# Kernel optimization log

Hardware: AMD Instinct MI355X
Metric: run time of the kernel (lower is better)

The kernel has to match this reference:

```python
import jax, jax.numpy as jnp
import numpy as np

HEADS = 16
DIM = 1024
D_K = DIM // HEADS
SEQ = 2048


def setup_inputs() -> dict:
    key = jax.random.key(0)
    ks = jax.random.split(key, 11)
    s = 1.0 / np.sqrt(DIM).astype(np.float32)
    return {
        "q": jax.random.normal(ks[0], (SEQ, DIM), jnp.float32),
        "k": jax.random.normal(ks[1], (SEQ, DIM), jnp.float32),
        "v": jax.random.normal(ks[2], (SEQ, DIM), jnp.float32),
        "Wq": jax.random.normal(ks[3], (DIM, DIM), jnp.float32) * s,
        "bq": jax.random.normal(ks[4], (DIM,), jnp.float32) * 0.01,
        "Wk": jax.random.normal(ks[5], (DIM, DIM), jnp.float32) * s,
        "bk": jax.random.normal(ks[6], (DIM,), jnp.float32) * 0.01,
        "Wv": jax.random.normal(ks[7], (DIM, DIM), jnp.float32) * s,
        "bv": jax.random.normal(ks[8], (DIM,), jnp.float32) * 0.01,
        "Wo": jax.random.normal(ks[9], (DIM, DIM), jnp.float32) * s,
        "bo": jax.random.normal(ks[10], (DIM,), jnp.float32) * 0.01,
    }


def reference(q, k, v, Wq, bq, Wk, bk, Wv, bv, Wo, bo):
    S = q.shape[0]
    # torch Linear: x @ W.T + b; view to (1, S, H, d_k) then transpose to (1, H, S, d_k)
    def proj(x, W, b):
        return (x @ W.T + b).reshape(1, S, HEADS, D_K).transpose(0, 2, 1, 3)

    qh = proj(q, Wq, bq)  # (1, H, S, d)
    kh = proj(k, Wk, bk)
    vh = proj(v, Wv, bv)

    scale = 1.0 / np.sqrt(D_K).astype(np.float32)
    scores = jnp.einsum("bhqd,bhkd->bhqk", qh, kh) * scale  # (1, H, S, S)
    # NOTE: source applies softmax over dim=1 == the HEADS axis (faithful quirk)
    attn = jax.nn.softmax(scores, axis=1)
    ctx = jnp.einsum("bhqk,bhkd->bhqd", attn, vh)  # (1, H, S, d)
    concat = ctx.transpose(0, 2, 1, 3).reshape(1, S, DIM)
    return concat @ Wo.T + bo
```

## Files before the change

kernel.cpp:

```cpp
#include <hip/hip_runtime.h>
#include <hip/hip_fp16.h>


typedef _Float16 f16;
typedef _Float16 f16x4 __attribute__((ext_vector_type(4)));
typedef _Float16 f16x8 __attribute__((ext_vector_type(8)));
typedef float    f32x4 __attribute__((ext_vector_type(4)));

#define S_LEN 2048
#define DIM   1024
#define NH    16
#define DK    64
#define EXP2K 0.1803368801111244f

#define MFMA(a, b, c) __builtin_amdgcn_mfma_f32_16x16x32_f16(a, b, c, 0, 0, 0)

#define VM_WAIT0   asm volatile("s_waitcnt vmcnt(0)" ::: "memory")
#define LGKM_WAIT0 asm volatile("s_waitcnt lgkmcnt(0)" ::: "memory")
#define WG_BARRIER asm volatile("s_barrier" ::: "memory")

typedef __attribute__((address_space(1))) void g_void;
typedef __attribute__((address_space(3))) void l_void;

static __device__ __forceinline__ void gload_lds16(const void* g, void* l) {
  __builtin_amdgcn_global_load_lds((g_void*)g, (l_void*)l, 16, 0, 0);
}

static __device__ __forceinline__ float exp_s(float s) {
  return __builtin_amdgcn_exp2f(s * EXP2K);
}

__global__ __launch_bounds__(256) void cvt_all(
    const float* __restrict__ q, const float* __restrict__ k, const float* __restrict__ v,
    const float* __restrict__ Wq, const float* __restrict__ Wk, const float* __restrict__ Wv,
    const float* __restrict__ Wo, f16* __restrict__ qh, f16* __restrict__ kh,
    f16* __restrict__ vh, f16* __restrict__ wqh, f16* __restrict__ wkh,
    f16* __restrict__ wvh, f16* __restrict__ woh) {
  const size_t M = 1048576;
  const int seg = blockIdx.y;
  const float* src;
  f16* dst;
  switch (seg) {
    case 0: src = q;      dst = qh;      break;
    case 1: src = q + M;  dst = qh + M;  break;
    case 2: src = k;      dst = kh;      break;
    case 3: src = k + M;  dst = kh + M;  break;
    case 4: src = v;      dst = vh;      break;
    case 5: src = v + M;  dst = vh + M;  break;
    case 6: src = Wq;     dst = wqh;     break;
    case 7: src = Wk;     dst = wkh;     break;
    case 8: src = Wv;     dst = wvh;     break;
    default: src = Wo;    dst = woh;     break;
  }
  int i = blockIdx.x * 256 + threadIdx.x;
  float4 vv = ((const float4*)src)[i];
  f16x4 o = {(f16)vv.x, (f16)vv.y, (f16)vv.z, (f16)vv.w};
  ((f16x4*)dst)[i] = o;
}

static __device__ __forceinline__ void gemm64_core(const f16* __restrict__ X,
                                                   const f16* __restrict__ W,
                                                   int bm, int bn,
                                                   f16* As, f16* Bs,
                                                   f32x4 (&acc)[4][2]) {
  const int tid = threadIdx.x;
  const int wv = tid >> 6;
  const int lane = tid & 63;
  const int qd = lane >> 4;
  const int l16 = lane & 15;
  const int wm = (wv & 1) * 64;
  const int wn = (wv >> 1) * 32;
  const int lr8 = lane >> 3, lc8 = lane & 7;
  const int l7 = l16 & 7;

  const f16* gA = X + (size_t)(bm + wv * 32 + lr8) * DIM + (lc8 ^ lr8) * 8;
  const f16* gB = W + (size_t)(bn + wv * 16 + lr8) * DIM + (lc8 ^ lr8) * 8;

  auto issue = [&](int t, f16* dA, f16* dB) {
#pragma unroll
    for (int g = 0; g < 4; g++)
      gload_lds16(gA + (size_t)(g * 8) * DIM + t * 64, dA + (wv * 32 + g * 8) * 64);
#pragma unroll
    for (int g = 0; g < 2; g++)
      gload_lds16(gB + (size_t)(g * 8) * DIM + t * 64, dB + (wv * 16 + g * 8) * 64);
  };

  issue(0, As, Bs);

#pragma unroll 2
  for (int t = 0; t < 16; t++) {
    const int buf = t & 1;
    VM_WAIT0;
    WG_BARRIER;
    if (t + 1 < 16)
      issue(t + 1, As + (buf ^ 1) * (128 * 64), Bs + (buf ^ 1) * (64 * 64));
    const f16* A = As + buf * (128 * 64);
    const f16* B = Bs + buf * (64 * 64);
#pragma unroll
    for (int kk = 0; kk < 2; kk++) {
      const int slot = ((kk * 4 + qd) ^ l7) * 8;
      f16x8 bf[2];
#pragma unroll
      for (int ni = 0; ni < 2; ni++)
        bf[ni] = *(const f16x8*)&B[(wn + ni * 16 + l16) * 64 + slot];
#pragma unroll
      for (int mi = 0; mi < 4; mi++) {
        f16x8 af = *(const f16x8*)&A[(wm + mi * 16 + l16) * 64 + slot];
#pragma unroll
        for (int ni = 0; ni < 2; ni++)
          acc[mi][ni] = MFMA(af, bf[ni], acc[mi][ni]);
      }
    }
  }
}

__global__ __launch_bounds__(256) void gemm_qkv(
    const f16* __restrict__ X0, const f16* __restrict__ X1, const f16* __restrict__ X2,
    const f16* __restrict__ W0, const f16* __restrict__ W1, const f16* __restrict__ W2,
    const float* __restrict__ b0, const float* __restrict__ b1, const float* __restrict__ b2,
    f16* __restrict__ o0, f16* __restrict__ o1, f16* __restrict__ o2) {
  __shared__ __align__(16) f16 As[2 * 128 * 64];
  __shared__ __align__(16) f16 Bs[2 * 64 * 64];
  const int z = blockIdx.z;
  const f16* X = z == 0 ? X0 : z == 1 ? X1 : X2;
  const f16* W = z == 0 ? W0 : z == 1 ? W1 : W2;
  const float* bias = z == 0 ? b0 : z == 1 ? b1 : b2;
  f16* outh = z == 0 ? o0 : z == 1 ? o1 : o2;

  const int bm = blockIdx.y * 128, bn = blockIdx.x * 64;
  f32x4 acc[4][2];
#pragma unroll
  for (int a = 0; a < 4; a++)
#pragma unroll
    for (int b = 0; b < 2; b++) acc[a][b] = (f32x4){0.f, 0.f, 0.f, 0.f};

  gemm64_core(X, W, bm, bn, As, Bs, acc);

  const int tid = threadIdx.x;
  const int wv = tid >> 6, lane = tid & 63;
  const int qd = lane >> 4, l16 = lane & 15;
  const int wm = (wv & 1) * 64, wn = (wv >> 1) * 32;
#pragma unroll
  for (int mi = 0; mi < 4; mi++) {
#pragma unroll
    for (int ni = 0; ni < 2; ni++) {
      const int gm = bm + wm + mi * 16 + qd * 4;
      const int gn = bn + wn + ni * 16 + l16;
      const float bs = bias[gn];
      if (z == 2) {
        f16x4 o = {(f16)(acc[mi][ni][0] + bs), (f16)(acc[mi][ni][1] + bs),
                   (f16)(acc[mi][ni][2] + bs), (f16)(acc[mi][ni][3] + bs)};
        const int pj = (gm & ~31) + ((gm >> 2) & 3) * 8 + ((gm >> 4) & 1) * 4;
        *(f16x4*)&outh[(size_t)gn * S_LEN + pj] = o;
      } else {
#pragma unroll
        for (int r = 0; r < 4; r++)
          outh[(size_t)(gm + r) * DIM + gn] = (f16)(acc[mi][ni][r] + bs);
      }
    }
  }
}

__global__ __launch_bounds__(256) void gemm_out(const f16* __restrict__ C0,
                                                const f16* __restrict__ C1,
                                                const f16* __restrict__ W,
                                                const float* __restrict__ bias,
                                                float* __restrict__ outf) {
  __shared__ __align__(16) f16 As[2 * 64 * 64];
  __shared__ __align__(16) f16 Bs[2 * 64 * 64];
  const int tid = threadIdx.x;
  const int wv = tid >> 6;
  const int lane = tid & 63;
  const int qd = lane >> 4;
  const int l16 = lane & 15;
  const int wm = (wv & 1) * 32;
  const int wn = (wv >> 1) * 32;
  const int lr8 = lane >> 3, lc8 = lane & 7;
  const int l7 = l16 & 7;
  const int bm = blockIdx.y * 64, bn = blockIdx.x * 64;

  const f16* gA0 = C0 + (size_t)(bm + wv * 16 + lr8) * DIM + lc8 * 8;
  const f16* gA1 = C1 + (size_t)(bm + wv * 16 + lr8) * DIM + lc8 * 8;
  const f16* gB  = W + (size_t)(bn + wv * 16 + lr8) * DIM + (lc8 ^ lr8) * 8;

  f16x8 a0[2], a1[2];
  auto issueA = [&](int t) {
#pragma unroll
    for (int g = 0; g < 2; g++) {
      a0[g] = *(const f16x8*)(gA0 + (size_t)(g * 8) * DIM + t * 64);
      a1[g] = *(const f16x8*)(gA1 + (size_t)(g * 8) * DIM + t * 64);
    }
  };
  auto issueB = [&](int t, f16* dB) {
#pragma unroll
    for (int g = 0; g < 2; g++)
      gload_lds16(gB + (size_t)(g * 8) * DIM + t * 64, dB + (wv * 16 + g * 8) * 64);
  };

  f32x4 acc[2][2];
#pragma unroll
  for (int a = 0; a < 2; a++)
#pragma unroll
    for (int b = 0; b < 2; b++) acc[a][b] = (f32x4){0.f, 0.f, 0.f, 0.f};

  issueA(0);
  issueB(0, Bs);

#pragma unroll 2
  for (int t = 0; t < 16; t++) {
    const int buf = t & 1;
    VM_WAIT0;
    f16* Ab = As + buf * (64 * 64);
#pragma unroll
    for (int g = 0; g < 2; g++) {
      f16x8 s;
#pragma unroll
      for (int j = 0; j < 8; j++) s[j] = (f16)((float)a0[g][j] + (float)a1[g][j]);
      *(f16x8*)&Ab[(wv * 16 + g * 8 + lr8) * 64 + (lc8 ^ lr8) * 8] = s;
    }
    LGKM_WAIT0;
    WG_BARRIER;
    if (t + 1 < 16) {
      issueA(t + 1);
      issueB(t + 1, Bs + (buf ^ 1) * (64 * 64));
    }
    const f16* A = Ab;
    const f16* B = Bs + buf * (64 * 64);
#pragma unroll
    for (int kk = 0; kk < 2; kk++) {
      const int slot = ((kk * 4 + qd) ^ l7) * 8;
      f16x8 bf[2], af[2];
#pragma unroll
      for (int ni = 0; ni < 2; ni++)
        bf[ni] = *(const f16x8*)&B[(wn + ni * 16 + l16) * 64 + slot];
#pragma unroll
      for (int mi = 0; mi < 2; mi++)
        af[mi] = *(const f16x8*)&A[(wm + mi * 16 + l16) * 64 + slot];
#pragma unroll
      for (int mi = 0; mi < 2; mi++)
#pragma unroll
        for (int ni = 0; ni < 2; ni++)
          acc[mi][ni] = MFMA(af[mi], bf[ni], acc[mi][ni]);
    }
  }

#pragma unroll
  for (int mi = 0; mi < 2; mi++) {
#pragma unroll
    for (int ni = 0; ni < 2; ni++) {
      const int gm = bm + wm + mi * 16 + qd * 4;
      const int gn = bn + wn + ni * 16 + l16;
      const float bs = bias[gn];
#pragma unroll
      for (int r = 0; r < 4; r++)
        outf[(size_t)(gm + r) * DIM + gn] = acc[mi][ni][r] + bs;
    }
  }
}

__global__ __launch_bounds__(256) void attn_denom(const f16* __restrict__ Qp,
                                                  const f16* __restrict__ Kp,
                                                  f16* __restrict__ IDn) {
  __shared__ __align__(16) f16 Qs[2][2][64 * 32];
  __shared__ __align__(16) f16 Ks[2][2][64 * 32];
  const int tid = threadIdx.x;
  const int wv = tid >> 6;
  const int lane = tid & 63;
  const int qd = lane >> 4;
  const int l16 = lane & 15;
  const int wm = (wv & 1) * 32, wn = (wv >> 1) * 32;
  const int flat = blockIdx.x + (blockIdx.y << 5);
  const int nf = ((flat & 7) << 7) + (flat >> 3);
  const int bi = (nf >> 5) * 64, bj = (nf & 31) * 64;
  const int lr4 = lane >> 2, lc4 = lane & 3;
  const int kkw = wv & 1;
  const int q0 = (wv >> 1) * 2;
  const int ssw = (lc4 ^ ((lr4 >> 1) & 3)) * 8;
  const int rsw = (qd ^ ((l16 >> 1) & 3)) * 8;

  f32x4 dsum[2][2];
#pragma unroll
  for (int a = 0; a < 2; a++)
#pragma unroll
    for (int b = 0; b < 2; b++) dsum[a][b] = (f32x4){0.f, 0.f, 0.f, 0.f};

  {
    const f16* gq = Qp + (size_t)(bi + q0 * 16 + lr4) * DIM + kkw * 32 + ssw;
    const f16* gk = Kp + (size_t)(bj + q0 * 16 + lr4) * DIM + kkw * 32 + ssw;
#pragma unroll
    for (int t = 0; t < 2; t++) {
      gload_lds16(gq + (size_t)t * 16 * DIM, &Qs[0][kkw][(q0 + t) * 16 * 32]);
      gload_lds16(gk + (size_t)t * 16 * DIM, &Ks[0][kkw][(q0 + t) * 16 * 32]);
    }
  }

#pragma unroll 2
  for (int h = 0; h < NH; h++) {
    const int buf = h & 1;
    VM_WAIT0;
    WG_BARRIER;
    if (h + 1 < NH) {
      const f16* gq = Qp + (size_t)(bi + q0 * 16 + lr4) * DIM + (h + 1) * DK + kkw * 32 + ssw;
      const f16* gk = Kp + (size_t)(bj + q0 * 16 + lr4) * DIM + (h + 1) * DK + kkw * 32 + ssw;
#pragma unroll
      for (int t = 0; t < 2; t++) {
        gload_lds16(gq + (size_t)t * 16 * DIM, &Qs[buf ^ 1][kkw][(q0 + t) * 16 * 32]);
        gload_lds16(gk + (size_t)t * 16 * DIM, &Ks[buf ^ 1][kkw][(q0 + t) * 16 * 32]);
      }
    }

#pragma unroll
    for (int mi = 0; mi < 2; mi++) {
      f16x8 af0 = *(const f16x8*)&Qs[buf][0][(wm + mi * 16 + l16) * 32 + rsw];
      f16x8 af1 = *(const f16x8*)&Qs[buf][1][(wm + mi * 16 + l16) * 32 + rsw];
#pragma unroll
      for (int ni = 0; ni < 2; ni++) {
        f16x8 bf0 = *(const f16x8*)&Ks[buf][0][(wn + ni * 16 + l16) * 32 + rsw];
        f16x8 bf1 = *(const f16x8*)&Ks[buf][1][(wn + ni * 16 + l16) * 32 + rsw];
        f32x4 s = {0.f, 0.f, 0.f, 0.f};
        s = MFMA(af0, bf0, s);
        s = MFMA(af1, bf1, s);
#pragma unroll
        for (int r = 0; r < 4; r++) dsum[mi][ni][r] += exp_s(s[r]);
      }
    }
  }
#pragma unroll
  for (int mi = 0; mi < 2; mi++)
#pragma unroll
    for (int ni = 0; ni < 2; ni++)
#pragma unroll
      for (int r = 0; r < 4; r++) {
        const int gi = bi + wm + mi * 16 + qd * 4 + r;
        const int gj = bj + wn + ni * 16 + l16;
        const int pj = (gj & ~31) + ((gj >> 2) & 3) * 8 + ((gj >> 4) & 1) * 4 + (gj & 3);
        IDn[(size_t)gi * S_LEN + pj] = (f16)(1.f / dsum[mi][ni][r]);
      }
}

__global__ __launch_bounds__(256, 4) void attn_ctx(const f16* __restrict__ Qp,
                                                   const f16* __restrict__ Kp,
                                                   const f16* __restrict__ Vt,
                                                   const f16* __restrict__ IDn,
                                                   f16* __restrict__ C0,
                                                   f16* __restrict__ C1) {
  __shared__ __align__(16) f16 Ks[2][2][64 * 32];
  __shared__ __align__(16) f16 Vs[2][64 * 64];
  const int tid = threadIdx.x;
  const int wv = tid >> 6;
  const int lane = tid & 63;
  const int qd = lane >> 4;
  const int l16 = lane & 15;
  const int flat = blockIdx.x + (blockIdx.y << 5) + (blockIdx.z << 9);
  const int nf = ((flat & 7) << 7) + (flat >> 3);
  const int h = (nf >> 5) & 15;
  const int iw = (nf & 31) * 64 + wv * 16;
  const int z = nf >> 9;
  const int jb = z * 1024;
  f16* Cz = z == 0 ? C0 : C1;
  const int lr4 = lane >> 2, lc4 = lane & 3;
  const int lr8 = lane >> 3, lc8 = lane & 7;
  const int kkw = wv & 1;
  const int rhw = wv >> 1;
  const int ssw = (lc4 ^ ((lr4 >> 1) & 3)) * 8;
  const int rsw = (qd ^ ((l16 >> 1) & 3)) * 8;
  const int l7 = l16 & 7;

  f16x8 aq[2];
#pragma unroll
  for (int kk = 0; kk < 2; kk++)
    aq[kk] = *(const f16x8*)(Qp + (size_t)(iw + l16) * DIM + h * DK + kk * 32 + qd * 8);

  f32x4 acc[4];
#pragma unroll
  for (int b = 0; b < 4; b++) acc[b] = (f32x4){0.f, 0.f, 0.f, 0.f};

  f16x8 idn[2][2];

  auto issue = [&](int tt, int pb) {
    const int j1 = jb + tt * 64;
    const f16* gk = Kp + (size_t)(j1 + rhw * 16 + lr4) * DIM + h * DK + kkw * 32 + ssw;
    gload_lds16(gk, &Ks[pb][kkw][(rhw * 16) * 32]);
    gload_lds16(gk + (size_t)32 * DIM, &Ks[pb][kkw][(rhw * 16 + 32) * 32]);
    const f16* gv = Vt + (size_t)(h * DK + wv * 16 + lr8) * S_LEN + j1 + (lc8 ^ lr8) * 8;
    gload_lds16(gv, &Vs[pb][(wv * 16) * 64]);
    gload_lds16(gv + (size_t)8 * S_LEN, &Vs[pb][(wv * 16 + 8) * 64]);
#pragma unroll
    for (int js = 0; js < 2; js++)
      idn[pb][js] = *(const f16x8*)(IDn + (size_t)(iw + l16) * S_LEN + j1 + js * 32 + qd * 8);
  };

  issue(0, 0);

#pragma unroll 2
  for (int t = 0; t < 16; t++) {
    const int buf = t & 1;
    VM_WAIT0;
    WG_BARRIER;
    if (t + 1 < 16) issue(t + 1, buf ^ 1);

    f16x8 pa[2];
#pragma unroll
    for (int js = 0; js < 2; js++) {
      f16x8 bk0[2], bk1[2];
#pragma unroll
      for (int kk = 0; kk < 2; kk++) {
        bk0[kk] = *(const f16x8*)&Ks[buf][kk][((js * 2) * 16 + l16) * 32 + rsw];
        bk1[kk] = *(const f16x8*)&Ks[buf][kk][((js * 2 + 1) * 16 + l16) * 32 + rsw];
      }
      f32x4 st0 = {0.f, 0.f, 0.f, 0.f};
      f32x4 st1 = {0.f, 0.f, 0.f, 0.f};
      st0 = MFMA(bk0[0], aq[0], st0);
      st0 = MFMA(bk0[1], aq[1], st0);
      st1 = MFMA(bk1[0], aq[0], st1);
      st1 = MFMA(bk1[1], aq[1], st1);
      f16x8 p;
#pragma unroll
      for (int r = 0; r < 4; r++) p[r] = (f16)(exp_s(st0[r]) * (float)idn[buf][js][r]);
#pragma unroll
      for (int r = 0; r < 4; r++) p[4 + r] = (f16)(exp_s(st1[r]) * (float)idn[buf][js][4 + r]);
      pa[js] = p;
    }

#pragma unroll
    for (int js = 0; js < 2; js++) {
#pragma unroll
      for (int nd = 0; nd < 4; nd++) {
        f16x8 bv = *(const f16x8*)&Vs[buf][(nd * 16 + l16) * 64 +
                                          (((js * 4 + qd) ^ l7) * 8)];
        acc[nd] = MFMA(pa[js], bv, acc[nd]);
      }
    }
  }

#pragma unroll
  for (int nd = 0; nd < 4; nd++)
#pragma unroll
    for (int r = 0; r < 4; r++)
      Cz[(size_t)(iw + qd * 4 + r) * DIM + h * DK + nd * 16 + l16] = (f16)acc[nd][r];
}

extern "C" void kernel_launch(void* const* d_in, const int* in_sizes, int n_in,
                              void* d_out, int out_size, void* d_ws, size_t ws_size,
                              hipStream_t stream) {
  const float* q  = (const float*)d_in[0];
  const float* k  = (const float*)d_in[1];
  const float* v  = (const float*)d_in[2];
  const float* Wq = (const float*)d_in[3];
  const float* bq = (const float*)d_in[4];
  const float* Wk = (const float*)d_in[5];
  const float* bk = (const float*)d_in[6];
  const float* Wv = (const float*)d_in[7];
  const float* bv = (const float*)d_in[8];
  const float* Wo = (const float*)d_in[9];
  const float* bo = (const float*)d_in[10];
  float* out = (float*)d_out;

  f16* w = (f16*)d_ws;
  f16* qh  = w;
  f16* kh  = qh + (size_t)S_LEN * DIM;
  f16* vh  = kh + (size_t)S_LEN * DIM;
  f16* wqh = vh + (size_t)S_LEN * DIM;
  f16* wkh = wqh + (size_t)DIM * DIM;
  f16* wvh = wkh + (size_t)DIM * DIM;
  f16* woh = wvh + (size_t)DIM * DIM;
  f16* Qp  = woh + (size_t)DIM * DIM;
  f16* Kp  = Qp + (size_t)S_LEN * DIM;
  f16* Vt  = Kp + (size_t)S_LEN * DIM;
  f16* IDn = qh;
  f16* C0  = vh;
  f16* C1  = wqh;

  dim3 b256(256);
  cvt_all<<<dim3(1024, 10), b256, 0, stream>>>(q, k, v, Wq, Wk, Wv, Wo,
                                               qh, kh, vh, wqh, wkh, wvh, woh);

  gemm_qkv<<<dim3(DIM / 64, S_LEN / 128, 3), b256, 0, stream>>>(
      qh, kh, vh, wqh, wkh, wvh, bq, bk, bv, Qp, Kp, Vt);

  attn_denom<<<dim3(S_LEN / 64, S_LEN / 64), b256, 0, stream>>>(Qp, Kp, IDn);
  attn_ctx<<<dim3(S_LEN / 64, NH, 2), b256, 0, stream>>>(Qp, Kp, Vt, IDn, C0, C1);

  gemm_out<<<dim3(DIM / 64, S_LEN / 64), b256, 0, stream>>>(C0, C1, woh, bo, out);
}
```

Measured before the change: 194.8 us.

## Swizzle GEMM block order and load attention Q fragments directly into registers

Both projection GEMMs now remap their flat block index so that consecutive blocks spread across tiles in a grouped order, aiming for better L2 reuse across XCDs. In attn_denom, the Q tile is no longer staged through LDS. Each wave loads its Q MFMA fragments straight from global memory into double-buffered registers, and the kernel gets a launch_bounds occupancy hint of 4. This removes Q's LDS traffic and halves shared memory use, at the cost of more registers and uncoalesced-ish direct global loads.

```diff
diff --git a/kernel.cpp b/kernel.cpp
--- a/kernel.cpp
+++ b/kernel.cpp
@@ -121,13 +121,16 @@
     f16* __restrict__ o0, f16* __restrict__ o1, f16* __restrict__ o2) {
   __shared__ __align__(16) f16 As[2 * 128 * 64];
   __shared__ __align__(16) f16 Bs[2 * 64 * 64];
-  const int z = blockIdx.z;
+  const int flat = blockIdx.x + (blockIdx.y << 4) + (blockIdx.z << 8);
+  const int nfq = (flat & 7) * 96 + (flat >> 3);
+  const int z = nfq >> 8;
+  const int bm = ((nfq >> 4) & 15) * 128;
+  const int bn = (nfq & 15) * 64;
   const f16* X = z == 0 ? X0 : z == 1 ? X1 : X2;
   const f16* W = z == 0 ? W0 : z == 1 ? W1 : W2;
   const float* bias = z == 0 ? b0 : z == 1 ? b1 : b2;
   f16* outh = z == 0 ? o0 : z == 1 ? o1 : o2;
 
-  const int bm = blockIdx.y * 128, bn = blockIdx.x * 64;
   f32x4 acc[4][2];
 #pragma unroll
   for (int a = 0; a < 4; a++)
@@ -177,7 +180,9 @@
   const int wn = (wv >> 1) * 32;
   const int lr8 = lane >> 3, lc8 = lane & 7;
   const int l7 = l16 & 7;
-  const int bm = blockIdx.y * 64, bn = blockIdx.x * 64;
+  const int flat = blockIdx.x + (blockIdx.y << 4);
+  const int nfo = ((flat & 7) << 6) + (flat >> 3);
+  const int bm = (nfo >> 4) * 64, bn = (nfo & 15) * 64;
 
   const f16* gA0 = C0 + (size_t)(bm + wv * 16 + lr8) * DIM + lc8 * 8;
   const f16* gA1 = C1 + (size_t)(bm + wv * 16 + lr8) * DIM + lc8 * 8;
@@ -258,10 +263,9 @@
   }
 }
 
-__global__ __launch_bounds__(256) void attn_denom(const f16* __restrict__ Qp,
-                                                  const f16* __restrict__ Kp,
-                                                  f16* __restrict__ IDn) {
-  __shared__ __align__(16) f16 Qs[2][2][64 * 32];
+__global__ __launch_bounds__(256, 4) void attn_denom(const f16* __restrict__ Qp,
+                                                     const f16* __restrict__ Kp,
+                                                     f16* __restrict__ IDn) {
   __shared__ __align__(16) f16 Ks[2][2][64 * 32];
   const int tid = threadIdx.x;
   const int wv = tid >> 6;
@@ -284,15 +288,22 @@
 #pragma unroll
     for (int b = 0; b < 2; b++) dsum[a][b] = (f32x4){0.f, 0.f, 0.f, 0.f};
 
+  f16x8 afr[2][2][2];
+  auto loadQ = [&](int hh, int pb) {
+#pragma unroll
+    for (int mi = 0; mi < 2; mi++)
+#pragma unroll
+      for (int kk = 0; kk < 2; kk++)
+        afr[pb][mi][kk] = *(const f16x8*)(Qp + (size_t)(bi + wm + mi * 16 + l16) * DIM +
+                                          hh * DK + kk * 32 + qd * 8);
+  };
+
   {
-    const f16* gq = Qp + (size_t)(bi + q0 * 16 + lr4) * DIM + kkw * 32 + ssw;
     const f16* gk = Kp + (size_t)(bj + q0 * 16 + lr4) * DIM + kkw * 32 + ssw;
-#pragma unroll
-    for (int t = 0; t < 2; t++) {
-      gload_lds16(gq + (size_t)t * 16 * DIM, &Qs[0][kkw][(q0 + t) * 16 * 32]);
-      gload_lds16(gk + (size_t)t * 16 * DIM, &Ks[0][kkw][(q0 + t) * 16 * 32]);
-    }
-  }
+    gload_lds16(gk, &Ks[0][kkw][(q0) * 16 * 32]);
+    gload_lds16(gk + (size_t)16 * DIM, &Ks[0][kkw][(q0 + 1) * 16 * 32]);
+  }
+  loadQ(0, 0);
 
 #pragma unroll 2
   for (int h = 0; h < NH; h++) {
@@ -300,19 +311,16 @@
     VM_WAIT0;
     WG_BARRIER;
     if (h + 1 < NH) {
-      const f16* gq = Qp + (size_t)(bi + q0 * 16 + lr4) * DIM + (h + 1) * DK + kkw * 32 + ssw;
       const f16* gk = Kp + (size_t)(bj + q0 * 16 + lr4) * DIM + (h + 1) * DK + kkw * 32 + ssw;
-#pragma unroll
-      for (int t = 0; t < 2; t++) {
-        gload_lds16(gq + (size_t)t * 16 * DIM, &Qs[buf ^ 1][kkw][(q0 + t) * 16 * 32]);
-        gload_lds16(gk + (size_t)t * 16 * DIM, &Ks[buf ^ 1][kkw][(q0 + t) * 16 * 32]);
-      }
+      gload_lds16(gk, &Ks[buf ^ 1][kkw][(q0) * 16 * 32]);
+      gload_lds16(gk + (size_t)16 * DIM, &Ks[buf ^ 1][kkw][(q0 + 1) * 16 * 32]);
+      loadQ(h + 1, buf ^ 1);
     }
 
 #pragma unroll
     for (int mi = 0; mi < 2; mi++) {
-      f16x8 af0 = *(const f16x8*)&Qs[buf][0][(wm + mi * 16 + l16) * 32 + rsw];
-      f16x8 af1 = *(const f16x8*)&Qs[buf][1][(wm + mi * 16 + l16) * 32 + rsw];
+      f16x8 af0 = afr[buf][mi][0];
+      f16x8 af1 = afr[buf][mi][1];
 #pragma unroll
       for (int ni = 0; ni < 2; ni++) {
         f16x8 bf0 = *(const f16x8*)&Ks[buf][0][(wn + ni * 16 + l16) * 32 + rsw];
```

Result: slower. 205.9 us (+5.7%).
